# Performance work log

Measured on AMD Instinct MI355X. Metric: run time of the kernel, lower is better.

Reference implementation:

```python
import jax, jax.numpy as jnp
import numpy as np

B, T, C, H = 2, 2048, 1024, 16


def setup_inputs() -> dict:
    key = jax.random.key(0)
    ks = jax.random.split(key, 9)
    s = 1.0 / np.sqrt(C)
    return {
        "query": jax.random.normal(ks[0], (B, T, C), dtype=jnp.float32),
        "Wq": jax.random.normal(ks[1], (C, C), dtype=jnp.float32) * s,
        "bq": jnp.zeros((C,), dtype=jnp.float32),
        "Wk": jax.random.normal(ks[2], (C, C), dtype=jnp.float32) * s,
        "bk": jnp.zeros((C,), dtype=jnp.float32),
        "Wv": jax.random.normal(ks[3], (C, C), dtype=jnp.float32) * s,
        "bv": jnp.zeros((C,), dtype=jnp.float32),
        "Wp": jax.random.normal(ks[4], (C, C), dtype=jnp.float32) * s,
        "bp": jnp.zeros((C,), dtype=jnp.float32),
        "n_head": H,
    }


def reference(query, Wq, bq, Wk, bk, Wv, bv, Wp, bp, n_head):
    b, t, c = query.shape
    d = c // n_head
    # QKV projections -> [b, h, t, d]
    q = (query @ Wq + bq).reshape(b, t, n_head, d).transpose(0, 2, 1, 3)
    k = (query @ Wk + bk).reshape(b, t, n_head, d).transpose(0, 2, 1, 3)
    v = (query @ Wv + bv).reshape(b, t, n_head, d).transpose(0, 2, 1, 3)
    scale = 1.0 / jnp.sqrt(jnp.asarray(d, dtype=query.dtype))
    att = jnp.einsum('bhtd,bhsd->bhts', q, k) * scale  # [b,h,t,t]
    causal = jnp.tril(jnp.ones((t, t), dtype=bool))
    att = jnp.where(causal[None, None, :, :], att, -jnp.inf)
    att = jax.nn.softmax(att, axis=-1)
    y = jnp.einsum('bhts,bhsd->bhtd', att, v)  # [b,h,t,d]
    y = y.transpose(0, 2, 1, 3).reshape(b, t, c)
    return y @ Wp + bp
```

## Files before the change

### kernel.cpp

```cpp
#include <hip/hip_runtime.h>
#include <math.h>

#define B_ 2
#define T_ 2048
#define C_ 1024
#define H_ 16
#define D_ 64
#define M_ (B_*T_)

typedef __bf16 bf16x8 __attribute__((ext_vector_type(8)));
typedef __bf16 bf16x4 __attribute__((ext_vector_type(4)));
typedef float  f32x4  __attribute__((ext_vector_type(4)));

__device__ __forceinline__ unsigned short f2bf(float f) {
    unsigned int u = __float_as_uint(f);
    u += 0x7FFFu + ((u >> 16) & 1u);
    return (unsigned short)(u >> 16);
}

__device__ __forceinline__ void gload16(const void* g, void* l) {
    __builtin_amdgcn_global_load_lds(
        (const __attribute__((address_space(1))) void*)g,
        (__attribute__((address_space(3))) void*)l, 16, 0, 0);
}

__global__ __launch_bounds__(256) void prep_kernel(
    const float* __restrict__ X, unsigned short* __restrict__ Xb,
    const float* __restrict__ W0, const float* __restrict__ W1,
    const float* __restrict__ W2, const float* __restrict__ W3,
    unsigned short* __restrict__ T0, unsigned short* __restrict__ T1,
    unsigned short* __restrict__ T2, unsigned short* __restrict__ T3)
{
    const int tid = threadIdx.x;
    if (blockIdx.x < 2048) {
        const size_t i = ((size_t)blockIdx.x * 256 + tid) * 8;
        const float4 a = *(const float4*)&X[i];
        const float4 b = *(const float4*)&X[i + 4];
        ushort4 s0, s1;
        s0.x = f2bf(a.x); s0.y = f2bf(a.y); s0.z = f2bf(a.z); s0.w = f2bf(a.w);
        s1.x = f2bf(b.x); s1.y = f2bf(b.y); s1.z = f2bf(b.z); s1.w = f2bf(b.w);
        *(ushort4*)&Xb[i]     = s0;
        *(ushort4*)&Xb[i + 4] = s1;
        return;
    }
    const int bz = blockIdx.x - 2048;
    const int z = bz >> 10, rem = bz & 1023;
    const float* W; unsigned short* Wt;
    switch (z) {
        case 0: W = W0; Wt = T0; break;
        case 1: W = W1; Wt = T1; break;
        case 2: W = W2; Wt = T2; break;
        default: W = W3; Wt = T3; break;
    }
    __shared__ unsigned short tile[32][33];
    const int k0 = (rem >> 5) * 32, n0 = (rem & 31) * 32;
    {
        const int r = tid >> 3, c = (tid & 7) * 4;
        const float4 v = *(const float4*)&W[(size_t)(k0 + r)*C_ + n0 + c];
        tile[c+0][r] = f2bf(v.x);
        tile[c+1][r] = f2bf(v.y);
        tile[c+2][r] = f2bf(v.z);
        tile[c+3][r] = f2bf(v.w);
    }
    __syncthreads();
    {
        const int r = tid >> 3, c = (tid & 7) * 4;
        ushort4 s;
        s.x = tile[r][c+0]; s.y = tile[r][c+1]; s.z = tile[r][c+2]; s.w = tile[r][c+3];
        *(ushort4*)&Wt[(size_t)(n0 + r)*C_ + k0 + c] = s;
    }
}

__global__ __launch_bounds__(256) void gemm_mfma_kernel(
    const unsigned short* __restrict__ A, const unsigned short* __restrict__ Bt,
    const float* __restrict__ b0, const float* __restrict__ b1,
    const float* __restrict__ b2,
    void* __restrict__ out0, void* __restrict__ out1, void* __restrict__ out2,
    int mode)
{
    __shared__ __align__(16) unsigned short Als[2][128 * 32];
    __shared__ __align__(16) unsigned short Bls[2][128 * 32];

    const int tid  = threadIdx.x;
    const int lane = tid & 63;
    const int wave = tid >> 6;
    const int wm = wave >> 1, wn = wave & 1;
    const int l15 = lane & 15, quad = lane >> 4;
    const int m0 = blockIdx.y * 128, n0 = blockIdx.x * 128;
    const int srow = lane >> 2;
    const int scol = (lane & 3) * 8;

    const f32x4 zero4 = {0.f, 0.f, 0.f, 0.f};
    f32x4 acc[4][4];
    #pragma unroll
    for (int i = 0; i < 4; ++i)
        #pragma unroll
        for (int j = 0; j < 4; ++j) acc[i][j] = zero4;

    for (int k0 = 0; k0 < C_; k0 += 64) {
        __syncthreads();
        #pragma unroll
        for (int h = 0; h < 2; ++h) {
            #pragma unroll
            for (int u = 0; u < 2; ++u) {
                const int r = wave*32 + u*16 + srow;
                gload16(&A [(size_t)(m0 + r)*C_ + k0 + h*32 + scol],
                        &Als[h][(wave*32 + u*16)*32]);
                gload16(&Bt[(size_t)(n0 + r)*C_ + k0 + h*32 + scol],
                        &Bls[h][(wave*32 + u*16)*32]);
            }
        }
        __syncthreads();

        #pragma unroll
        for (int h = 0; h < 2; ++h) {
            bf16x8 af[4], bfr[4];
            #pragma unroll
            for (int i = 0; i < 4; ++i)
                af[i] = *(const bf16x8*)&Als[h][(wm*64 + i*16 + l15)*32 + quad*8];
            #pragma unroll
            for (int j = 0; j < 4; ++j)
                bfr[j] = *(const bf16x8*)&Bls[h][(wn*64 + j*16 + l15)*32 + quad*8];

            #pragma unroll
            for (int i = 0; i < 4; ++i)
                #pragma unroll
                for (int j = 0; j < 4; ++j)
                    acc[i][j] = __builtin_amdgcn_mfma_f32_16x16x32_bf16(
                        af[i], bfr[j], acc[i][j], 0, 0, 0);
        }
    }

    if (mode == 0) {
        float* o0 = (float*)out0;
        #pragma unroll
        for (int j = 0; j < 4; ++j) {
            const int n = n0 + wn*64 + j*16 + l15;
            const float bias = b0[n];
            #pragma unroll
            for (int i = 0; i < 4; ++i)
                #pragma unroll
                for (int r = 0; r < 4; ++r) {
                    const int m = m0 + wm*64 + i*16 + quad*4 + r;
                    o0[(size_t)m*C_ + n] = acc[i][j][r] + bias;
                }
        }
        return;
    }

    __syncthreads();
    unsigned short* Ep = (wave < 2) ? &Als[wave][0] : &Bls[wave - 2][0];

    const int which = n0 >> 10;
    const int c0 = n0 & (C_ - 1);
    const int h  = (c0 >> 6) + wn;
    const int bb = m0 >> 11;
    const int t0 = (m0 & (T_ - 1)) + wm*64;
    const int bh = bb*H_ + h;
    const float* bp = (which == 0) ? b0 : (which == 1 ? b1 : b2);
    const float qscale = (which == 0) ? 0.125f : 1.0f;

    if (which < 2) {
        #pragma unroll
        for (int j = 0; j < 4; ++j) {
            const int cl = j*16 + l15;
            const float bias = bp[c0 + wn*64 + cl];
            #pragma unroll
            for (int i = 0; i < 4; ++i)
                #pragma unroll
                for (int r = 0; r < 4; ++r)
                    Ep[(i*16 + quad*4 + r)*64 + cl] =
                        f2bf((acc[i][j][r] + bias) * qscale);
        }
        unsigned short* op = (which == 0) ? (unsigned short*)out0
                                          : (unsigned short*)out1;
        const int chunk = lane & 7;
        #pragma unroll
        for (int u = 0; u < 8; ++u) {
            const int row = u*8 + (lane >> 3);
            const uint4 v = *(const uint4*)&Ep[row*64 + chunk*8];
            *(uint4*)&op[((size_t)bh*T_ + t0 + row)*D_ + chunk*8] = v;
        }
    } else {
        #pragma unroll
        for (int j = 0; j < 4; ++j) {
            const int cl = j*16 + l15;
            const float bias = bp[c0 + wn*64 + cl];
            const int xo = (l15 & 7) * 8;
            #pragma unroll
            for (int i = 0; i < 4; ++i) {
                ushort4 pk;
                pk.x = f2bf(acc[i][j][0] + bias);
                pk.y = f2bf(acc[i][j][1] + bias);
                pk.z = f2bf(acc[i][j][2] + bias);
                pk.w = f2bf(acc[i][j][3] + bias);
                *(ushort4*)&Ep[cl*64 + ((i*16 + quad*4) ^ xo)] = pk;
            }
        }
        unsigned short* op = (unsigned short*)out2;
        const int chunk = lane & 7;
        #pragma unroll
        for (int u = 0; u < 8; ++u) {
            const int d = u*8 + (lane >> 3);
            const uint4 v = *(const uint4*)&Ep[d*64 + ((chunk*8) ^ ((d & 7)*8))];
            *(uint4*)&op[((size_t)bh*D_ + d)*T_ + t0 + chunk*8] = v;
        }
    }
}

__global__ __launch_bounds__(512, 2) void gemm256_qkv_kernel(
    const unsigned short* __restrict__ A, const unsigned short* __restrict__ Bt,
    const float* __restrict__ b0, const float* __restrict__ b1,
    const float* __restrict__ b2,
    unsigned short* __restrict__ outq, unsigned short* __restrict__ outk,
    unsigned short* __restrict__ outv)
{
    __shared__ __align__(16) unsigned short lds[4 * 16384];

    const int tid  = threadIdx.x;
    const int lane = tid & 63;
    const int wave = tid >> 6;
    const int l15  = lane & 15, quad = lane >> 4;
    const int wm   = wave >> 2, wn = wave & 3;
    const int m0   = blockIdx.y * 256, n0 = blockIdx.x * 256;

    const int lrow = lane >> 2;
    const int csw  = ((lane & 3) ^ ((lane >> 3) & 3)) * 8;
    const int sw8  = (quad ^ ((l15 >> 1) & 3)) * 8;

#define STAGE(tt) do {                                                         \
        const int bi_ = ((tt) & 3) << 14;                                      \
        const int k0_ = (tt) << 5;                                             \
        const int ra_ = m0 + wave*32 + lrow;                                   \
        const int rb_ = n0 + wave*32 + lrow;                                   \
        gload16(&A [(size_t)ra_*C_ + k0_ + csw],      &lds[bi_ + wave*1024]);  \
        gload16(&Bt[(size_t)rb_*C_ + k0_ + csw],      &lds[bi_ + 8192 + wave*1024]); \
        gload16(&A [(size_t)(ra_+16)*C_ + k0_ + csw], &lds[bi_ + wave*1024 + 512]);  \
        gload16(&Bt[(size_t)(rb_+16)*C_ + k0_ + csw], &lds[bi_ + 8192 + wave*1024 + 512]); \
    } while (0)

    const f32x4 zero4 = {0.f, 0.f, 0.f, 0.f};
    f32x4 acc[8][4];
    #pragma unroll
    for (int i = 0; i < 8; ++i)
        #pragma unroll
        for (int j = 0; j < 4; ++j) acc[i][j] = zero4;

    STAGE(0); STAGE(1); STAGE(2);

    for (int t = 0; t < 32; ++t) {
        const int bi = (t & 3) << 14;
        __builtin_amdgcn_s_barrier();
        __builtin_amdgcn_sched_barrier(0);
        if (t < 29) {
            STAGE(t + 3);
            asm volatile("s_waitcnt vmcnt(12)" ::: "memory");
        } else if (t == 29) {
            asm volatile("s_waitcnt vmcnt(8)" ::: "memory");
        } else if (t == 30) {
            asm volatile("s_waitcnt vmcnt(4)" ::: "memory");
        } else {
            asm volatile("s_waitcnt vmcnt(0)" ::: "memory");
        }
        __builtin_amdgcn_s_barrier();
        __builtin_amdgcn_sched_barrier(0);

        const unsigned short* Ab = &lds[bi];
        const unsigned short* Bb = &lds[bi + 8192];

        bf16x8 bfr[4], af[4];
        #pragma unroll
        for (int j = 0; j < 4; ++j)
            bfr[j] = *(const bf16x8*)&Bb[(wn*64 + j*16 + l15)*32 + sw8];
        #pragma unroll
        for (int i = 0; i < 4; ++i)
            af[i] = *(const bf16x8*)&Ab[(wm*128 + i*16 + l15)*32 + sw8];

        __builtin_amdgcn_s_setprio(1);
        #pragma unroll
        for (int i = 0; i < 4; ++i)
            #pragma unroll
            for (int j = 0; j < 4; ++j)
                acc[i][j] = __builtin_amdgcn_mfma_f32_16x16x32_bf16(
                    af[i], bfr[j], acc[i][j], 0, 0, 0);
        __builtin_amdgcn_s_setprio(0);

        #pragma unroll
        for (int i = 0; i < 4; ++i)
            af[i] = *(const bf16x8*)&Ab[(wm*128 + 64 + i*16 + l15)*32 + sw8];

        __builtin_amdgcn_s_setprio(1);
        #pragma unroll
        for (int i = 0; i < 4; ++i)
            #pragma unroll
            for (int j = 0; j < 4; ++j)
                acc[4+i][j] = __builtin_amdgcn_mfma_f32_16x16x32_bf16(
                    af[i], bfr[j], acc[4+i][j], 0, 0, 0);
        __builtin_amdgcn_s_setprio(0);
    }
#undef STAGE

    __syncthreads();

    unsigned short* Ep = &lds[wave * 8192];
    const int which = n0 >> 10;
    const int c0 = (n0 & 1023) + wn * 64;
    const int h  = c0 >> 6;
    const int bb = m0 >> 11;
    const int t0 = (m0 & (T_ - 1)) + wm * 128;
    const int bh = bb * H_ + h;
    const float* bp = (which == 0) ? b0 : (which == 1 ? b1 : b2);
    const float qscale = (which == 0) ? 0.125f : 1.0f;

    if (which < 2) {
        __bf16* Eb = (__bf16*)Ep;
        #pragma unroll
        for (int j = 0; j < 4; ++j) {
            const int cl = j*16 + l15;
            const float bias = bp[c0 + cl];
            #pragma unroll
            for (int i = 0; i < 8; ++i)
                #pragma unroll
                for (int r = 0; r < 4; ++r)
                    Eb[(i*16 + quad*4 + r)*64 + cl] =
                        (__bf16)((acc[i][j][r] + bias) * qscale);
        }
        unsigned short* op = (which == 0) ? outq : outk;
        const int row8 = lane >> 3, chunk = lane & 7;
        #pragma unroll
        for (int u = 0; u < 16; ++u) {
            const int row = u*8 + row8;
            const uint4 v = *(const uint4*)&Ep[row*64 + chunk*8];
            *(uint4*)&op[((size_t)bh*T_ + t0 + row)*D_ + chunk*8] = v;
        }
    } else {
        #pragma unroll
        for (int j = 0; j < 4; ++j) {
            const int cl = j*16 + l15;
            const float bias = bp[c0 + cl];
            const int xo = (cl & 7) * 8;
            #pragma unroll
            for (int i = 0; i < 8; ++i) {
                bf16x4 pk = {(__bf16)(acc[i][j][0] + bias),
                             (__bf16)(acc[i][j][1] + bias),
                             (__bf16)(acc[i][j][2] + bias),
                             (__bf16)(acc[i][j][3] + bias)};
                *(bf16x4*)&Ep[cl*128 + ((i*16 + quad*4) ^ xo)] = pk;
            }
        }
        const int d4 = lane >> 4, chunk = lane & 15;
        #pragma unroll
        for (int u = 0; u < 16; ++u) {
            const int d = u*4 + d4;
            const uint4 v = *(const uint4*)&Ep[d*128 + ((chunk*8) ^ ((d & 7)*8))];
            *(uint4*)&outv[((size_t)bh*D_ + d)*T_ + t0 + chunk*8] = v;
        }
    }
}

__global__ __launch_bounds__(256) void flash_mfma_kernel(
    const unsigned short* __restrict__ Qs, const unsigned short* __restrict__ Ks,
    const unsigned short* __restrict__ Vts, unsigned short* __restrict__ Y,
    float* __restrict__ parts, float* __restrict__ lbase)
{
    __shared__ __align__(16) unsigned short Kls[64 * 64];
    __shared__ __align__(16) unsigned short Vls[64 * 64];
    __shared__ __align__(16) unsigned short Pls[4 * 2048];

    const int tid  = threadIdx.x;
    const int lane = tid & 63, wave = tid >> 6;
    const int l15  = lane & 15, quad = lane >> 4;
    const int job  = blockIdx.x >> 5;
    const int bh   = blockIdx.x & 31;
    const bool isA = (job < 8);
    const int a    = isA ? job : job - 8;

    int qts[2], slos[2], shis[2], slots[2], nseg;
    if (isA) {
        qts[0] = a;      slos[0] = 0;        shis[0] = 2*a + 2;  slots[0] = -1;
        qts[1] = 15 - a; slos[1] = 0;        shis[1] = 15 - 2*a; slots[1] = 0;
        nseg = 2;
    } else {
        qts[0] = 15 - a; slos[0] = 15 - 2*a; shis[0] = 32 - 2*a; slots[0] = 1;
        nseg = 1;
    }

    unsigned short* Pw = &Pls[wave * 2048];
    const int kd_s = wave >> 1;
    const int c8_s = (kd_s * 4 + quad) * 8;
    const int b_ = bh >> 4, h_ = bh & (H_ - 1);
    const f32x4 zero4 = {0.f, 0.f, 0.f, 0.f};

    for (int sg = 0; sg < nseg; ++sg) {
        const int qt  = qts[sg];
        const int qw0 = qt * 128 + wave * 32;

        bf16x8 qf[2][2];
        #pragma unroll
        for (int i = 0; i < 2; ++i)
            #pragma unroll
            for (int kd = 0; kd < 2; ++kd)
                qf[i][kd] = *(const bf16x8*)&Qs[((size_t)bh*T_ + qw0 + i*16 + l15)*D_
                                                + kd*32 + quad*8];

        f32x4 o[2][4];
        #pragma unroll
        for (int i = 0; i < 2; ++i)
            #pragma unroll
            for (int jd = 0; jd < 4; ++jd) o[i][jd] = zero4;
        float lsum[2] = {0.f, 0.f};

        for (int it = slos[sg]; it < shis[sg]; ++it) {
            const int s0 = it * 64;
            __syncthreads();
            #pragma unroll
            for (int u = 0; u < 2; ++u) {
                const int cu  = 2*wave + u;
                const int row = ((cu & 3) << 4) + l15;
                gload16(&Ks [((size_t)bh*T_ + s0 + row)*D_ + c8_s],
                        (char*)Kls + cu*1024);
                gload16(&Vts[((size_t)bh*D_ + row)*T_ + s0 + c8_s],
                        (char*)Vls + cu*1024);
            }
            __syncthreads();

            if (s0 > qw0 + 31) continue;

            f32x4 st[2][4];
            #pragma unroll
            for (int i = 0; i < 2; ++i)
                #pragma unroll
                for (int j = 0; j < 4; ++j) st[i][j] = zero4;
            #pragma unroll
            for (int kd = 0; kd < 2; ++kd) {
                bf16x8 kf[4];
                #pragma unroll
                for (int j = 0; j < 4; ++j)
                    kf[j] = *(const bf16x8*)&Kls[lane*8 + j*512 + kd*2048];
                #pragma unroll
                for (int i = 0; i < 2; ++i)
                    #pragma unroll
                    for (int j = 0; j < 4; ++j)
                        st[i][j] = __builtin_amdgcn_mfma_f32_16x16x32_bf16(
                            kf[j], qf[i][kd], st[i][j], 0, 0, 0);
            }

            const bool diag = (s0 + 63 > qw0);
            #pragma unroll
            for (int i = 0; i < 2; ++i) {
                const int qrow = qw0 + i*16 + l15;
                #pragma unroll
                for (int j = 0; j < 4; ++j)
                    #pragma unroll
                    for (int r = 0; r < 4; ++r) {
                        float e = __expf(st[i][j][r]);
                        if (diag && (s0 + j*16 + quad*4 + r > qrow)) e = 0.f;
                        st[i][j][r] = e;
                        lsum[i] += e;
                    }
            }

            #pragma unroll
            for (int i = 0; i < 2; ++i)
                #pragma unroll
                for (int j = 0; j < 4; ++j) {
                    bf16x4 pk = {(__bf16)st[i][j][0], (__bf16)st[i][j][1],
                                 (__bf16)st[i][j][2], (__bf16)st[i][j][3]};
                    *(bf16x4*)&Pw[(((j>>1)*2 + i)*4 + (j&1)*2 + (quad>>1))*128
                                   + l15*8 + (quad&1)*4] = pk;
                }

            #pragma unroll
            for (int kk = 0; kk < 2; ++kk) {
                bf16x8 pf[2], vf[4];
                #pragma unroll
                for (int i = 0; i < 2; ++i)
                    pf[i] = *(const bf16x8*)&Pw[(kk*2 + i)*512 + lane*8];
                #pragma unroll
                for (int jd = 0; jd < 4; ++jd)
                    vf[jd] = *(const bf16x8*)&Vls[lane*8 + jd*512 + kk*2048];
                #pragma unroll
                for (int i = 0; i < 2; ++i)
                    #pragma unroll
                    for (int jd = 0; jd < 4; ++jd)
                        o[i][jd] = __builtin_amdgcn_mfma_f32_16x16x32_bf16(
                            vf[jd], pf[i], o[i][jd], 0, 0, 0);
            }
        }

        #pragma unroll
        for (int i = 0; i < 2; ++i) {
            float v = lsum[i];
            v += __shfl_xor(v, 16, 64);
            v += __shfl_xor(v, 32, 64);
            lsum[i] = v;
        }

        if (slots[sg] < 0) {
            #pragma unroll
            for (int i = 0; i < 2; ++i) {
                const float inv = 1.0f / lsum[i];
                const int t = qw0 + i*16 + l15;
                #pragma unroll
                for (int jd = 0; jd < 4; ++jd) {
                    bf16x4 pk = {(__bf16)(o[i][jd][0] * inv),
                                 (__bf16)(o[i][jd][1] * inv),
                                 (__bf16)(o[i][jd][2] * inv),
                                 (__bf16)(o[i][jd][3] * inv)};
                    *(bf16x4*)&Y[((size_t)(b_*T_ + t))*C_ + h_*D_ + jd*16 + quad*4]
                        = pk;
                }
            }
        } else {
            const int gpi = bh*16 + a*2 + slots[sg];
            float* Op = parts + (size_t)gpi*8192;
            float* Lp = lbase + gpi*128;
            #pragma unroll
            for (int i = 0; i < 2; ++i) {
                const int tl = wave*32 + i*16 + l15;
                if (quad == 0) Lp[tl] = lsum[i];
                #pragma unroll
                for (int jd = 0; jd < 4; ++jd)
                    *(f32x4*)&Op[(size_t)tl*64 + jd*16 + quad*4] = o[i][jd];
            }
        }
    }
}

__global__ __launch_bounds__(256) void merge_kernel(
    const float* __restrict__ parts, const float* __restrict__ lbase,
    unsigned short* __restrict__ Y)
{
    const int pair = blockIdx.x;
    const int bh = pair >> 3, p = pair & 7;
    const int qt = 15 - p;
    const int g0 = bh*16 + p*2;
    const float* O0 = parts + (size_t)g0*8192;
    const float* O1 = O0 + 8192;
    const float* L0 = lbase + g0*128;
    const float* L1 = L0 + 128;

    const int tid = threadIdx.x;
    const int r = tid >> 1, c0 = (tid & 1) * 32;
    const float inv = 1.0f / (L0[r] + L1[r]);
    const int b = bh >> 4, h = bh & (H_ - 1);
    const int t = qt*128 + r;
    #pragma unroll
    for (int k = 0; k < 8; ++k) {
        const f32x4 a  = *(const f32x4*)&O0[(size_t)r*64 + c0 + k*4];
        const f32x4 bb = *(const f32x4*)&O1[(size_t)r*64 + c0 + k*4];
        bf16x4 pk = {(__bf16)((a[0]+bb[0])*inv), (__bf16)((a[1]+bb[1])*inv),
                     (__bf16)((a[2]+bb[2])*inv), (__bf16)((a[3]+bb[3])*inv)};
        *(bf16x4*)&Y[((size_t)(b*T_ + t))*C_ + h*D_ + c0 + k*4] = pk;
    }
}

extern "C" void kernel_launch(void* const* d_in, const int* in_sizes, int n_in,
                              void* d_out, int out_size, void* d_ws, size_t ws_size,
                              hipStream_t stream) {
    const float* query = (const float*)d_in[0];
    const float* Wq = (const float*)d_in[1];
    const float* bq = (const float*)d_in[2];
    const float* Wk = (const float*)d_in[3];
    const float* bk = (const float*)d_in[4];
    const float* Wv = (const float*)d_in[5];
    const float* bv = (const float*)d_in[6];
    const float* Wp = (const float*)d_in[7];
    const float* bp = (const float*)d_in[8];
    float* out = (float*)d_out;

    char* ws = (char*)d_ws;
    unsigned short* qbf   = (unsigned short*)(ws);
    unsigned short* kbf   = (unsigned short*)(ws + 8388608);
    unsigned short* vtbf  = (unsigned short*)(ws + 16777216);
    unsigned short* WtP   = (unsigned short*)(ws + 25165824);
    unsigned short* WtQKV = (unsigned short*)(ws + 27262976);
    unsigned short* yb    = (unsigned short*)(ws + 33554432);
    unsigned short* qx    = (unsigned short*)(ws + 41943040);
    float* lbase = (float*)(ws + 27262976);
    float* parts = out;

    prep_kernel<<<6144, 256, 0, stream>>>(
        query, qx, Wq, Wk, Wv, Wp,
        WtQKV, WtQKV + (size_t)C_*C_, WtQKV + 2*(size_t)C_*C_, WtP);

    gemm256_qkv_kernel<<<dim3(12, 16), 512, 0, stream>>>(
        qx, WtQKV, bq, bk, bv, qbf, kbf, vtbf);

    flash_mfma_kernel<<<512, 256, 0, stream>>>(qbf, kbf, vtbf, yb, parts, lbase);
    merge_kernel<<<256, 256, 0, stream>>>(parts, lbase, yb);

    gemm_mfma_kernel<<<dim3(C_/128, M_/128), 256, 0, stream>>>(
        yb, WtP, bp, bp, bp, out, nullptr, nullptr, 0);
}
```

Baseline: 201.8 us.

## Double-buffer K/V tiles in flash kernel and switch softmax to exp2

The flash attention loop now keeps two LDS buffers for K and V. It issues the global-to-LDS loads for the next tile before computing on the current one, using explicit vmcnt waits and raw barriers instead of two __syncthreads per iteration. The Q scale folds in log2(e) so the softmax can use exp2f instead of __expf, and MFMA blocks are wrapped in s_setprio. This doubles K/V LDS use, which may lower occupancy, and the hand-written waitcnt/barrier scheme has to be exactly right to avoid races.

```diff
diff --git a/kernel.cpp b/kernel.cpp
--- a/kernel.cpp
+++ b/kernel.cpp
@@ -310,7 +310,7 @@
     const int t0 = (m0 & (T_ - 1)) + wm * 128;
     const int bh = bb * H_ + h;
     const float* bp = (which == 0) ? b0 : (which == 1 ? b1 : b2);
-    const float qscale = (which == 0) ? 0.125f : 1.0f;
+    const float qscale = (which == 0) ? 0.18033688f : 1.0f;
 
     if (which < 2) {
         __bf16* Eb = (__bf16*)Ep;
@@ -363,8 +363,8 @@
     const unsigned short* __restrict__ Vts, unsigned short* __restrict__ Y,
     float* __restrict__ parts, float* __restrict__ lbase)
 {
-    __shared__ __align__(16) unsigned short Kls[64 * 64];
-    __shared__ __align__(16) unsigned short Vls[64 * 64];
+    __shared__ __align__(16) unsigned short Kls[2][64 * 64];
+    __shared__ __align__(16) unsigned short Vls[2][64 * 64];
     __shared__ __align__(16) unsigned short Pls[4 * 2048];
 
     const int tid  = threadIdx.x;
@@ -391,6 +391,20 @@
     const int b_ = bh >> 4, h_ = bh & (H_ - 1);
     const f32x4 zero4 = {0.f, 0.f, 0.f, 0.f};
 
+#define FSTAGE(itv, bb_) do {                                                  \
+        const int s0_ = (itv) * 64;                                            \
+        const int r0_ = (((2*wave) & 3) << 4) + l15;                           \
+        const int r1_ = (((2*wave + 1) & 3) << 4) + l15;                       \
+        gload16(&Ks [((size_t)bh*T_ + s0_ + r0_)*D_ + c8_s],                   \
+                (char*)&Kls[bb_][0] + (2*wave)*1024);                          \
+        gload16(&Vts[((size_t)bh*D_ + r0_)*T_ + s0_ + c8_s],                   \
+                (char*)&Vls[bb_][0] + (2*wave)*1024);                          \
+        gload16(&Ks [((size_t)bh*T_ + s0_ + r1_)*D_ + c8_s],                   \
+                (char*)&Kls[bb_][0] + (2*wave + 1)*1024);                      \
+        gload16(&Vts[((size_t)bh*D_ + r1_)*T_ + s0_ + c8_s],                   \
+                (char*)&Vls[bb_][0] + (2*wave + 1)*1024);                      \
+    } while (0)
+
     for (int sg = 0; sg < nseg; ++sg) {
         const int qt  = qts[sg];
         const int qw0 = qt * 128 + wave * 32;
@@ -410,82 +424,91 @@
             for (int jd = 0; jd < 4; ++jd) o[i][jd] = zero4;
         float lsum[2] = {0.f, 0.f};
 
-        for (int it = slos[sg]; it < shis[sg]; ++it) {
+        const int lo = slos[sg], hi = shis[sg];
+        if (sg) __builtin_amdgcn_s_barrier();
+        FSTAGE(lo, 0);
+        int cur = 0;
+
+        for (int it = lo; it < hi; ++it) {
+            __builtin_amdgcn_s_barrier();
+            __builtin_amdgcn_sched_barrier(0);
+            if (it + 1 < hi) {
+                FSTAGE(it + 1, cur ^ 1);
+                asm volatile("s_waitcnt vmcnt(4)" ::: "memory");
+            } else {
+                asm volatile("s_waitcnt vmcnt(0)" ::: "memory");
+            }
+            __builtin_amdgcn_s_barrier();
+            __builtin_amdgcn_sched_barrier(0);
+
             const int s0 = it * 64;
-            __syncthreads();
-            #pragma unroll
-            for (int u = 0; u < 2; ++u) {
-                const int cu  = 2*wave + u;
-                const int row = ((cu & 3) << 4) + l15;
-                gload16(&Ks [((size_t)bh*T_ + s0 + row)*D_ + c8_s],
-                        (char*)Kls + cu*1024);
-                gload16(&Vts[((size_t)bh*D_ + row)*T_ + s0 + c8_s],
-                        (char*)Vls + cu*1024);
+            if (s0 <= qw0 + 31) {
+                f32x4 st[2][4];
+                #pragma unroll
+                for (int i = 0; i < 2; ++i)
+                    #pragma unroll
+                    for (int j = 0; j < 4; ++j) st[i][j] = zero4;
+                #pragma unroll
+                for (int kd = 0; kd < 2; ++kd) {
+                    bf16x8 kf[4];
+                    #pragma unroll
+                    for (int j = 0; j < 4; ++j)
+                        kf[j] = *(const bf16x8*)&Kls[cur][lane*8 + j*512 + kd*2048];
+                    __builtin_amdgcn_s_setprio(1);
+                    #pragma unroll
+                    for (int i = 0; i < 2; ++i)
+                        #pragma unroll
+                        for (int j = 0; j < 4; ++j)
+                            st[i][j] = __builtin_amdgcn_mfma_f32_16x16x32_bf16(
+                                kf[j], qf[i][kd], st[i][j], 0, 0, 0);
+                    __builtin_amdgcn_s_setprio(0);
+                }
+
+                const bool diag = (s0 + 63 > qw0);
+                #pragma unroll
+                for (int i = 0; i < 2; ++i) {
+                    const int qrow = qw0 + i*16 + l15;
+                    #pragma unroll
+                    for (int j = 0; j < 4; ++j)
+                        #pragma unroll
+                        for (int r = 0; r < 4; ++r) {
+                            float e = exp2f(st[i][j][r]);
+                            if (diag && (s0 + j*16 + quad*4 + r > qrow)) e = 0.f;
+                            st[i][j][r] = e;
+                            lsum[i] += e;
+                        }
+                }
+
+                #pragma unroll
+                for (int i = 0; i < 2; ++i)
+                    #pragma unroll
+                    for (int j = 0; j < 4; ++j) {
+                        bf16x4 pk = {(__bf16)st[i][j][0], (__bf16)st[i][j][1],
+                                     (__bf16)st[i][j][2], (__bf16)st[i][j][3]};
+                        *(bf16x4*)&Pw[(((j>>1)*2 + i)*4 + (j&1)*2 + (quad>>1))*128
+                                       + l15*8 + (quad&1)*4] = pk;
+                    }
+
+                #pragma unroll
+                for (int kk = 0; kk < 2; ++kk) {
+                    bf16x8 pf[2], vf[4];
+                    #pragma unroll
+                    for (int i = 0; i < 2; ++i)
+                        pf[i] = *(const bf16x8*)&Pw[(kk*2 + i)*512 + lane*8];
+                    #pragma unroll
+                    for (int jd = 0; jd < 4; ++jd)
+                        vf[jd] = *(const bf16x8*)&Vls[cur][lane*8 + jd*512 + kk*2048];
+                    __builtin_amdgcn_s_setprio(1);
+                    #pragma unroll
+                    for (int i = 0; i < 2; ++i)
+                        #pragma unroll
+                        for (int jd = 0; jd < 4; ++jd)
+                            o[i][jd] = __builtin_amdgcn_mfma_f32_16x16x32_bf16(
+                                vf[jd], pf[i], o[i][jd], 0, 0, 0);
+                    __builtin_amdgcn_s_setprio(0);
+                }
             }
-            __syncthreads();
-
-            if (s0 > qw0 + 31) continue;
-
-            f32x4 st[2][4];
-            #pragma unroll
-            for (int i = 0; i < 2; ++i)
-                #pragma unroll
-                for (int j = 0; j < 4; ++j) st[i][j] = zero4;
-            #pragma unroll
-            for (int kd = 0; kd < 2; ++kd) {
-                bf16x8 kf[4];
-                #pragma unroll
-                for (int j = 0; j < 4; ++j)
-                    kf[j] = *(const bf16x8*)&Kls[lane*8 + j*512 + kd*2048];
-                #pragma unroll
-                for (int i = 0; i < 2; ++i)
-                    #pragma unroll
-                    for (int j = 0; j < 4; ++j)
-                        st[i][j] = __builtin_amdgcn_mfma_f32_16x16x32_bf16(
-                            kf[j], qf[i][kd], st[i][j], 0, 0, 0);
-            }
-
-            const bool diag = (s0 + 63 > qw0);
-            #pragma unroll
-            for (int i = 0; i < 2; ++i) {
-                const int qrow = qw0 + i*16 + l15;
-                #pragma unroll
-                for (int j = 0; j < 4; ++j)
-                    #pragma unroll
-                    for (int r = 0; r < 4; ++r) {
-                        float e = __expf(st[i][j][r]);
-                        if (diag && (s0 + j*16 + quad*4 + r > qrow)) e = 0.f;
-                        st[i][j][r] = e;
-                        lsum[i] += e;
-                    }
-            }
-
-            #pragma unroll
-            for (int i = 0; i < 2; ++i)
-                #pragma unroll
-                for (int j = 0; j < 4; ++j) {
-                    bf16x4 pk = {(__bf16)st[i][j][0], (__bf16)st[i][j][1],
-                                 (__bf16)st[i][j][2], (__bf16)st[i][j][3]};
-                    *(bf16x4*)&Pw[(((j>>1)*2 + i)*4 + (j&1)*2 + (quad>>1))*128
-                                   + l15*8 + (quad&1)*4] = pk;
-                }
-
-            #pragma unroll
-            for (int kk = 0; kk < 2; ++kk) {
-                bf16x8 pf[2], vf[4];
-                #pragma unroll
-                for (int i = 0; i < 2; ++i)
-                    pf[i] = *(const bf16x8*)&Pw[(kk*2 + i)*512 + lane*8];
-                #pragma unroll
-                for (int jd = 0; jd < 4; ++jd)
-                    vf[jd] = *(const bf16x8*)&Vls[lane*8 + jd*512 + kk*2048];
-                #pragma unroll
-                for (int i = 0; i < 2; ++i)
-                    #pragma unroll
-                    for (int jd = 0; jd < 4; ++jd)
-                        o[i][jd] = __builtin_amdgcn_mfma_f32_16x16x32_bf16(
-                            vf[jd], pf[i], o[i][jd], 0, 0, 0);
-            }
+            cur ^= 1;
         }
 
         #pragma unroll
@@ -525,6 +548,7 @@
             }
         }
     }
+#undef FSTAGE
 }
 
 __global__ __launch_bounds__(256) void merge_kernel(
```

Measured after the change: 212.5 us. 5.3% more time.

## Load K/V fragments straight from global in flash kernel, drop LDS staging

Applied to the files above, without the earlier changes.

The flash attention kernel now reads K and V^T MFMA operand fragments directly from global memory into registers instead of cooperatively staging them in LDS. This removes two block-wide barriers per key tile and lets waves skip fully masked tiles before any load. It also folds log2(e) into the Q scale so the kernel can use exp2f instead of __expf, and raises wave priority around the MFMA blocks. In exchange each wave fetches its own copy of K/V from global or L2 with no reuse across waves, which adds memory traffic. Dead epilogue code in an unused GEMM path is also deleted.

```diff
diff --git a/kernel.cpp b/kernel.cpp
--- a/kernel.cpp
+++ b/kernel.cpp
@@ -147,65 +147,6 @@
         }
         return;
     }
-
-    __syncthreads();
-    unsigned short* Ep = (wave < 2) ? &Als[wave][0] : &Bls[wave - 2][0];
-
-    const int which = n0 >> 10;
-    const int c0 = n0 & (C_ - 1);
-    const int h  = (c0 >> 6) + wn;
-    const int bb = m0 >> 11;
-    const int t0 = (m0 & (T_ - 1)) + wm*64;
-    const int bh = bb*H_ + h;
-    const float* bp = (which == 0) ? b0 : (which == 1 ? b1 : b2);
-    const float qscale = (which == 0) ? 0.125f : 1.0f;
-
-    if (which < 2) {
-        #pragma unroll
-        for (int j = 0; j < 4; ++j) {
-            const int cl = j*16 + l15;
-            const float bias = bp[c0 + wn*64 + cl];
-            #pragma unroll
-            for (int i = 0; i < 4; ++i)
-                #pragma unroll
-                for (int r = 0; r < 4; ++r)
-                    Ep[(i*16 + quad*4 + r)*64 + cl] =
-                        f2bf((acc[i][j][r] + bias) * qscale);
-        }
-        unsigned short* op = (which == 0) ? (unsigned short*)out0
-                                          : (unsigned short*)out1;
-        const int chunk = lane & 7;
-        #pragma unroll
-        for (int u = 0; u < 8; ++u) {
-            const int row = u*8 + (lane >> 3);
-            const uint4 v = *(const uint4*)&Ep[row*64 + chunk*8];
-            *(uint4*)&op[((size_t)bh*T_ + t0 + row)*D_ + chunk*8] = v;
-        }
-    } else {
-        #pragma unroll
-        for (int j = 0; j < 4; ++j) {
-            const int cl = j*16 + l15;
-            const float bias = bp[c0 + wn*64 + cl];
-            const int xo = (l15 & 7) * 8;
-            #pragma unroll
-            for (int i = 0; i < 4; ++i) {
-                ushort4 pk;
-                pk.x = f2bf(acc[i][j][0] + bias);
-                pk.y = f2bf(acc[i][j][1] + bias);
-                pk.z = f2bf(acc[i][j][2] + bias);
-                pk.w = f2bf(acc[i][j][3] + bias);
-                *(ushort4*)&Ep[cl*64 + ((i*16 + quad*4) ^ xo)] = pk;
-            }
-        }
-        unsigned short* op = (unsigned short*)out2;
-        const int chunk = lane & 7;
-        #pragma unroll
-        for (int u = 0; u < 8; ++u) {
-            const int d = u*8 + (lane >> 3);
-            const uint4 v = *(const uint4*)&Ep[d*64 + ((chunk*8) ^ ((d & 7)*8))];
-            *(uint4*)&op[((size_t)bh*D_ + d)*T_ + t0 + chunk*8] = v;
-        }
-    }
 }
 
 __global__ __launch_bounds__(512, 2) void gemm256_qkv_kernel(
@@ -310,7 +251,7 @@
     const int t0 = (m0 & (T_ - 1)) + wm * 128;
     const int bh = bb * H_ + h;
     const float* bp = (which == 0) ? b0 : (which == 1 ? b1 : b2);
-    const float qscale = (which == 0) ? 0.125f : 1.0f;
+    const float qscale = (which == 0) ? 0.18033688f : 1.0f;
 
     if (which < 2) {
         __bf16* Eb = (__bf16*)Ep;
@@ -363,8 +304,6 @@
     const unsigned short* __restrict__ Vts, unsigned short* __restrict__ Y,
     float* __restrict__ parts, float* __restrict__ lbase)
 {
-    __shared__ __align__(16) unsigned short Kls[64 * 64];
-    __shared__ __align__(16) unsigned short Vls[64 * 64];
     __shared__ __align__(16) unsigned short Pls[4 * 2048];
 
     const int tid  = threadIdx.x;
@@ -386,10 +325,11 @@
     }
 
     unsigned short* Pw = &Pls[wave * 2048];
-    const int kd_s = wave >> 1;
-    const int c8_s = (kd_s * 4 + quad) * 8;
     const int b_ = bh >> 4, h_ = bh & (H_ - 1);
     const f32x4 zero4 = {0.f, 0.f, 0.f, 0.f};
+
+    const unsigned short* Kb = Ks  + ((size_t)bh*T_ + l15)*D_ + quad*8;
+    const unsigned short* Vb = Vts + ((size_t)bh*D_ + l15)*T_ + quad*8;
 
     for (int sg = 0; sg < nseg; ++sg) {
         const int qt  = qts[sg];
@@ -412,20 +352,24 @@
 
         for (int it = slos[sg]; it < shis[sg]; ++it) {
             const int s0 = it * 64;
-            __syncthreads();
-            #pragma unroll
-            for (int u = 0; u < 2; ++u) {
-                const int cu  = 2*wave + u;
-                const int row = ((cu & 3) << 4) + l15;
-                gload16(&Ks [((size_t)bh*T_ + s0 + row)*D_ + c8_s],
-                        (char*)Kls + cu*1024);
-                gload16(&Vts[((size_t)bh*D_ + row)*T_ + s0 + c8_s],
-                        (char*)Vls + cu*1024);
-            }
-            __syncthreads();
-
             if (s0 > qw0 + 31) continue;
 
+            bf16x8 kf[2][4];
+            const unsigned short* Kp = Kb + (size_t)s0 * D_;
+            #pragma unroll
+            for (int kd = 0; kd < 2; ++kd)
+                #pragma unroll
+                for (int j = 0; j < 4; ++j)
+                    kf[kd][j] = *(const bf16x8*)&Kp[(j*16)*D_ + kd*32];
+
+            bf16x8 vf[2][4];
+            const unsigned short* Vp = Vb + s0;
+            #pragma unroll
+            for (int kk = 0; kk < 2; ++kk)
+                #pragma unroll
+                for (int jd = 0; jd < 4; ++jd)
+                    vf[kk][jd] = *(const bf16x8*)&Vp[(jd*16)*T_ + kk*32];
+
             f32x4 st[2][4];
             #pragma unroll
             for (int i = 0; i < 2; ++i)
@@ -433,16 +377,14 @@
                 for (int j = 0; j < 4; ++j) st[i][j] = zero4;
             #pragma unroll
             for (int kd = 0; kd < 2; ++kd) {
-                bf16x8 kf[4];
-                #pragma unroll
-                for (int j = 0; j < 4; ++j)
-                    kf[j] = *(const bf16x8*)&Kls[lane*8 + j*512 + kd*2048];
+                __builtin_amdgcn_s_setprio(1);
                 #pragma unroll
                 for (int i = 0; i < 2; ++i)
                     #pragma unroll
                     for (int j = 0; j < 4; ++j)
                         st[i][j] = __builtin_amdgcn_mfma_f32_16x16x32_bf16(
-                            kf[j], qf[i][kd], st[i][j], 0, 0, 0);
+                            kf[kd][j], qf[i][kd], st[i][j], 0, 0, 0);
+                __builtin_amdgcn_s_setprio(0);
             }
 
             const bool diag = (s0 + 63 > qw0);
@@ -453,7 +395,7 @@
                 for (int j = 0; j < 4; ++j)
                     #pragma unroll
                     for (int r = 0; r < 4; ++r) {
-                        float e = __expf(st[i][j][r]);
+                        float e = exp2f(st[i][j][r]);
                         if (diag && (s0 + j*16 + quad*4 + r > qrow)) e = 0.f;
                         st[i][j][r] = e;
                         lsum[i] += e;
@@ -472,19 +414,18 @@
 
             #pragma unroll
             for (int kk = 0; kk < 2; ++kk) {
-                bf16x8 pf[2], vf[4];
+                bf16x8 pf[2];
                 #pragma unroll
                 for (int i = 0; i < 2; ++i)
                     pf[i] = *(const bf16x8*)&Pw[(kk*2 + i)*512 + lane*8];
-                #pragma unroll
-                for (int jd = 0; jd < 4; ++jd)
-                    vf[jd] = *(const bf16x8*)&Vls[lane*8 + jd*512 + kk*2048];
+                __builtin_amdgcn_s_setprio(1);
                 #pragma unroll
                 for (int i = 0; i < 2; ++i)
                     #pragma unroll
                     for (int jd = 0; jd < 4; ++jd)
                         o[i][jd] = __builtin_amdgcn_mfma_f32_16x16x32_bf16(
-                            vf[jd], pf[i], o[i][jd], 0, 0, 0);
+                            vf[kk][jd], pf[i], o[i][jd], 0, 0, 0);
+                __builtin_amdgcn_s_setprio(0);
             }
         }
 
```

Measured after the change: 230.4 us. +14.2%, slower.
